# Optimization experiments

Measured on AMD Instinct MI355X. Metric: run time of the kernel, lower is better.

The kernel has to match this reference:

```python
import jax, jax.numpy as jnp
import numpy as np

NUM_ROUTES = 32 * 6 * 6  # 1152
NUM_CAPS = 10
IN_DIM = 8
OUT_DIM = 16
NUM_ITERS = 3

def _conv(x, w, stride):
    return jax.lax.conv_general_dilated(
        x, w, window_strides=(stride, stride), padding='VALID',
        dimension_numbers=('NCHW', 'OIHW', 'NCHW'))

def _squash(u):
    # squash over last axis, exactly as torch code (no eps)
    sn = (u ** 2).sum(-1, keepdims=True)
    return sn * u / ((1.0 + sn) * jnp.sqrt(sn))

def setup_inputs() -> dict:
    key = jax.random.key(0)
    ks = jax.random.split(key, 10)
    B = 512
    data = jax.random.normal(ks[0], (B, 1, 28, 28), dtype=jnp.float32)
    conv_w = jax.random.normal(ks[1], (256, 1, 9, 9), dtype=jnp.float32) * 0.05
    conv_b = jnp.zeros((256,), dtype=jnp.float32)
    # 8 primary-capsule convs stacked caps-major -> fused conv [8*32,256,9,9]
    pc_w = jax.random.normal(ks[2], (8 * 32, 256, 9, 9), dtype=jnp.float32) * 0.01
    pc_b = jnp.zeros((8 * 32,), dtype=jnp.float32)
    W = jax.random.normal(ks[3], (NUM_ROUTES, NUM_CAPS, OUT_DIM, IN_DIM), dtype=jnp.float32)
    enc_w1 = jax.random.normal(ks[4], (512, OUT_DIM * NUM_CAPS), dtype=jnp.float32) * 0.05
    enc_b1 = jnp.zeros((512,), dtype=jnp.float32)
    enc_w2 = jax.random.normal(ks[5], (9, 512), dtype=jnp.float32) * 0.05
    enc_b2 = jnp.zeros((9,), dtype=jnp.float32)
    return dict(data=data, conv_w=conv_w, conv_b=conv_b, pc_w=pc_w, pc_b=pc_b,
                W=W, enc_w1=enc_w1, enc_b1=enc_b1, enc_w2=enc_w2, enc_b2=enc_b2)

def reference(data, conv_w, conv_b, pc_w, pc_b, W, enc_w1, enc_b1, enc_w2, enc_b2):
    B = data.shape[0]
    # ConvLayer: conv + relu -> [B,256,20,20]
    x = jax.nn.relu(_conv(data, conv_w, 1) + conv_b[None, :, None, None])
    # PrimaryCaps: 8 stride-2 convs (fused, caps-major channels) -> [B,256,6,6]
    u = _conv(x, pc_w, 2) + pc_b[None, :, None, None]
    # torch: stack(dim=1) then view(B, num_routes, -1) == reshape caps-major flat
    u = u.reshape(B, NUM_ROUTES, IN_DIM)
    u = _squash(u)  # [B,R,8]
    # WaferCaps: u_hat[b,r,c,o] = sum_i W[r,c,o,i] * u[b,r,i]
    u_hat = jnp.einsum('rcoi,bri->brco', W, u)  # [B,R,C,O]
    b_ij = jnp.zeros((NUM_ROUTES, NUM_CAPS), dtype=u_hat.dtype)
    v = None
    for it in range(NUM_ITERS):
        c_ij = jax.nn.softmax(b_ij, axis=0)  # softmax over routes (dim=1 in torch)
        s = jnp.einsum('rc,brco->bco', c_ij, u_hat)  # [B,C,O]
        # original squashes [B,1,C,O,1] over last (size-1) dim -> elementwise
        s2 = s ** 2
        v = s2 * s / ((1.0 + s2) * jnp.sqrt(s2))  # = s*|s|/(1+s^2)
        if it < NUM_ITERS - 1:
            a = jnp.einsum('brco,bco->brc', u_hat, v)  # [B,R,C]
            b_ij = b_ij + a.mean(axis=0)
    # Encoder: flatten [B,C,O] row-major -> [B,160]
    flat = v.reshape(B, NUM_CAPS * OUT_DIM)
    h = jax.nn.relu(flat @ enc_w1.T + enc_b1)  # dropout is identity at eval
    out = jax.nn.sigmoid(h @ enc_w2.T + enc_b2)
    return out
```

## Files before the change

### kernel.cpp

```cpp
#include <hip/hip_runtime.h>
#include <hip/hip_bf16.h>
#include <stdint.h>


typedef __bf16 bf16_t;
typedef __bf16 bf16x4 __attribute__((ext_vector_type(4)));
typedef __bf16 bf16x8 __attribute__((ext_vector_type(8)));
typedef float f32x4 __attribute__((ext_vector_type(4)));
typedef int i32x4 __attribute__((ext_vector_type(4)));
typedef int i32x8 __attribute__((ext_vector_type(8)));

__device__ __forceinline__ void gload_lds16(const void* g, void* l) {
    __builtin_amdgcn_global_load_lds((const __attribute__((address_space(1))) void*)g,
                                     (__attribute__((address_space(3))) void*)l, 16, 0, 0);
}

#define MEMBAR() asm volatile("" ::: "memory")

__device__ __forceinline__ uint8_t fp8b(float v) {
    return (uint8_t)(__builtin_amdgcn_cvt_pk_fp8_f32(v, 0.f, 0, false) & 0xFF);
}

__global__ void k_prep(const float* __restrict__ w1, const float* __restrict__ cw,
                       float* __restrict__ w1t, bf16_t* __restrict__ Bc1,
                       float* __restrict__ bij) {
    int blk = blockIdx.x, tid = threadIdx.x;
    if (blk < 45) {
        int i = blk * 256 + tid;
        if (i < 11520) bij[i] = 0.f;
    } else if (blk < 365) {
        int i = (blk - 45) * 256 + tid;
        int j = i / 160, k = i % 160;
        w1t[k * 512 + j] = w1[i];
    } else {
        int i = (blk - 365) * 256 + tid;
        if (i < 26624) {
            int oc = i / 104, k = i % 104;
            Bc1[i] = (k < 81) ? (bf16_t)cw[oc * 81 + k] : (bf16_t)0.f;
        }
    }
}

__global__ __launch_bounds__(256) void k_w2t(const float* __restrict__ pcw,
                                             uint8_t* __restrict__ w2t8) {
    __shared__ uint16_t tmp16[10368];
    int oc = blockIdx.x, tid = threadIdx.x;
    const float* src = pcw + (size_t)oc * 20736;
    for (int q2 = tid; q2 < 10368; q2 += 256) {
        float a = src[q2 * 2] * 64.f;
        float b = src[q2 * 2 + 1] * 64.f;
        uint32_t pk = __builtin_amdgcn_cvt_pk_fp8_f32(a, b, 0, false);
        tmp16[q2] = (uint16_t)(pk & 0xFFFF);
    }
    __syncthreads();
    uint32_t* dst = (uint32_t*)(w2t8 + (size_t)oc * 20736);
    for (int w = tid; w < 5184; w += 256) {
        int k = w * 4;
        int t = k >> 8, ic0 = k & 255;
        uint32_t r = 0;
#pragma unroll
        for (int j = 0; j < 4; ++j) {
            int s = (ic0 + j) * 81 + t;
            uint32_t b = (tmp16[s >> 1] >> ((s & 1) * 8)) & 0xFF;
            r |= b << (8 * j);
        }
        dst[w] = r;
    }
}

__global__ __launch_bounds__(512) void k_c1gemm(const float* __restrict__ data,
                                                const bf16_t* __restrict__ Bc1,
                                                const float* __restrict__ cb,
                                                uint8_t* __restrict__ xt8) {
    __shared__ __align__(16) bf16_t As[128 * 104];
    __shared__ __align__(16) bf16_t Bs[256 * 104];
    __shared__ float img[1568];
    int tid = threadIdx.x, lane = tid & 63, wave = tid >> 6;
    int wm = wave >> 2, wn = wave & 3;
    for (int i = tid; i < 3328; i += 512) {
        int byte = i * 16;
        int r = byte / 208;
        int c16 = (byte - r * 208) >> 4;
        gload_lds16(Bc1 + r * 104 + c16 * 8, (char*)Bs + byte);
    }
    int mr = wm * 64 + (lane & 15);
    int nr = wn * 64 + (lane & 15);
    float bias[4];
#pragma unroll
    for (int nj = 0; nj < 4; ++nj) bias[nj] = cb[nr + nj * 16];

    for (int t = 0; t < 2; ++t) {
        int m0 = (blockIdx.x + t * 800) * 128;
        int bfirst = m0 / 400;
        int blast = (m0 + 127) / 400;
        int nimg = blast - bfirst + 1;
        __syncthreads();
        for (int i = tid; i < nimg * 784; i += 512)
            img[i] = data[(size_t)bfirst * 784 + i];
        __syncthreads();
        for (int e = tid; e < 13312; e += 512) {
            int r = e / 104, k = e - r * 104;
            int m = m0 + r;
            int b = m / 400, pos = m - b * 400;
            int oh = pos / 20, ow = pos - oh * 20;
            float x = 0.f;
            if (k < 81) {
                int kh = k / 9, kw = k - kh * 9;
                x = img[(b - bfirst) * 784 + (oh + kh) * 28 + ow + kw];
            }
            As[e] = (bf16_t)x;
        }
        asm volatile("s_waitcnt vmcnt(0)" ::: "memory");
        __syncthreads();
        f32x4 acc[4][4];
#pragma unroll
        for (int mi = 0; mi < 4; ++mi)
#pragma unroll
            for (int nj = 0; nj < 4; ++nj) acc[mi][nj] = (f32x4){0.f, 0.f, 0.f, 0.f};
#pragma unroll
        for (int kk = 0; kk < 3; ++kk) {
            int ch = (kk * 4 + (lane >> 4)) * 8;
            bf16x8 af[4], bfr[4];
#pragma unroll
            for (int i = 0; i < 4; ++i) af[i] = *(const bf16x8*)&As[(mr + i * 16) * 104 + ch];
#pragma unroll
            for (int j = 0; j < 4; ++j) bfr[j] = *(const bf16x8*)&Bs[(nr + j * 16) * 104 + ch];
#pragma unroll
            for (int mi = 0; mi < 4; ++mi)
#pragma unroll
                for (int nj = 0; nj < 4; ++nj)
                    acc[mi][nj] = __builtin_amdgcn_mfma_f32_16x16x32_bf16(af[mi], bfr[nj], acc[mi][nj], 0, 0, 0);
        }
        int mbase = m0 + wm * 64 + (lane >> 4) * 4;
#pragma unroll
        for (int mi = 0; mi < 4; ++mi)
#pragma unroll
            for (int nj = 0; nj < 4; ++nj)
#pragma unroll
                for (int j = 0; j < 4; ++j)
                    xt8[(size_t)(mbase + mi * 16 + j) * 256 + nr + nj * 16] =
                        fp8b(fmaxf(acc[mi][nj][j] + bias[nj], 0.f));
    }
}

__global__ __launch_bounds__(256) void k_pcgemm(const uint8_t* __restrict__ xt8,
                                                const uint8_t* __restrict__ w2t8,
                                                bf16_t* __restrict__ parts) {
    __shared__ __align__(16) uint8_t As[128 * 128];
    __shared__ __align__(16) uint8_t Bs[128 * 128];
    int bid = blockIdx.x;
    int mt = bid % 144;
    int nt = (bid / 144) & 1;
    int ks = bid / 288;
    int m0 = mt * 128, n0 = nt * 128;
    int tid = threadIdx.x, lane = tid & 63, wave = tid >> 6;

    int csrc = (tid & 7) ^ ((tid >> 3) & 7);
    int arow[4];
#pragma unroll
    for (int p = 0; p < 4; ++p) {
        int m = m0 + p * 32 + (tid >> 3);
        int bb = m / 36, pos = m % 36;
        int oh = pos / 6, ow = pos % 6;
        arow[p] = ((bb * 20 + oh * 2) * 20 + ow * 2) * 256;
    }
    const uint8_t* bbase = w2t8 + (size_t)(n0 + (tid >> 3)) * 20736 + csrc * 16;

    f32x4 acc[4][4];
#pragma unroll
    for (int mi = 0; mi < 4; ++mi)
#pragma unroll
        for (int ni = 0; ni < 4; ++ni) acc[mi][ni] = (f32x4){0.f, 0.f, 0.f, 0.f};

    int g0 = ks * 54;
    int mr = (wave >> 1) * 64 + (lane & 15);
    int nr = (wave & 1) * 64 + (lane & 15);
    int rx = lane & 7;
    int c0 = (2 * (lane >> 4)) ^ rx;
    int c1 = (2 * (lane >> 4) + 1) ^ rx;

    for (int it = 0; it < 54; ++it) {
        int g = g0 + it;
        int t = g >> 1, icb = g & 1;
        int kh = t / 9, kw = t - (t / 9) * 9;
        int aoff = (kh * 20 + kw) * 256 + icb * 128 + csrc * 16;
#pragma unroll
        for (int p = 0; p < 4; ++p) {
            gload_lds16(xt8 + arow[p] + aoff, &As[p * 4096 + tid * 16]);
            gload_lds16(bbase + (size_t)p * 32 * 20736 + (size_t)g * 128, &Bs[p * 4096 + tid * 16]);
        }
        __syncthreads();
        i32x8 af[4], bfr[4];
#pragma unroll
        for (int i = 0; i < 4; ++i) {
            i32x4 lo = *(const i32x4*)&As[(mr + i * 16) * 128 + c0 * 16];
            i32x4 hi = *(const i32x4*)&As[(mr + i * 16) * 128 + c1 * 16];
            af[i][0] = lo[0]; af[i][1] = lo[1]; af[i][2] = lo[2]; af[i][3] = lo[3];
            af[i][4] = hi[0]; af[i][5] = hi[1]; af[i][6] = hi[2]; af[i][7] = hi[3];
        }
#pragma unroll
        for (int i = 0; i < 4; ++i) {
            i32x4 lo = *(const i32x4*)&Bs[(nr + i * 16) * 128 + c0 * 16];
            i32x4 hi = *(const i32x4*)&Bs[(nr + i * 16) * 128 + c1 * 16];
            bfr[i][0] = lo[0]; bfr[i][1] = lo[1]; bfr[i][2] = lo[2]; bfr[i][3] = lo[3];
            bfr[i][4] = hi[0]; bfr[i][5] = hi[1]; bfr[i][6] = hi[2]; bfr[i][7] = hi[3];
        }
#pragma unroll
        for (int mi = 0; mi < 4; ++mi)
#pragma unroll
            for (int ni = 0; ni < 4; ++ni)
                acc[mi][ni] = __builtin_amdgcn_mfma_scale_f32_16x16x128_f8f6f4(
                    af[mi], bfr[ni], acc[mi][ni], 0, 0, 0, 0x7F7F7F7F, 0, 0x79797979);
        __syncthreads();
    }

    bf16_t* out = parts + (size_t)ks * 4718592;
    int mbase = m0 + (wave >> 1) * 64 + (lane >> 4) * 4;
    int nbase = n0 + (wave & 1) * 64 + (lane & 15);
#pragma unroll
    for (int mi = 0; mi < 4; ++mi)
#pragma unroll
        for (int ni = 0; ni < 4; ++ni)
#pragma unroll
            for (int j = 0; j < 4; ++j)
                out[(size_t)(mbase + mi * 16 + j) * 256 + nbase + ni * 16] = (bf16_t)acc[mi][ni][j];
}

__global__ __launch_bounds__(256) void k_squash(const bf16_t* __restrict__ parts,
                                                const float* __restrict__ pcb,
                                                bf16_t* __restrict__ ub) {
    __shared__ float s[36 * 257];
    int b = blockIdx.x, tid = threadIdx.x;
    for (int i = tid; i < 9216; i += 256) {
        float a = pcb[i & 255];
#pragma unroll
        for (int p = 0; p < 3; ++p) a += (float)parts[(size_t)p * 4718592 + (size_t)b * 9216 + i];
        s[(i >> 8) * 257 + (i & 255)] = a;
    }
    __syncthreads();
    for (int r = tid; r < 1152; r += 256) {
        int flat0 = r * 8;
        float val[8], sn = 0.f;
#pragma unroll
        for (int e = 0; e < 8; ++e) {
            int f = flat0 + e;
            float x = s[(f % 36) * 257 + f / 36];
            val[e] = x;
            sn += x * x;
        }
        float scale = sn / ((1.f + sn) * sqrtf(sn));
        bf16x8 vv;
#pragma unroll
        for (int e = 0; e < 8; ++e) vv[e] = (bf16_t)(val[e] * scale);
        *(bf16x8*)&ub[(size_t)b * 9216 + flat0] = vv;
    }
}

__global__ __launch_bounds__(256) void k_uT(const bf16_t* __restrict__ ub, bf16_t* __restrict__ uT) {
    __shared__ bf16_t t[64 * 66];
    int kt = blockIdx.x % 144, bt = blockIdx.x / 144;
    int k0 = kt * 64, b0 = bt * 64;
    int tid = threadIdx.x;
    int c8 = tid & 7;
#pragma unroll
    for (int p = 0; p < 2; ++p) {
        int r = p * 32 + (tid >> 3);
        bf16x8 vv = *(const bf16x8*)&ub[(size_t)(b0 + r) * 9216 + k0 + c8 * 8];
        uint32_t u4[4];
        *(bf16x8*)u4 = vv;
#pragma unroll
        for (int j2 = 0; j2 < 4; ++j2)
            *(uint32_t*)&t[r * 66 + c8 * 8 + j2 * 2] = u4[j2];
    }
    __syncthreads();
#pragma unroll
    for (int p = 0; p < 2; ++p) {
        int kp = p * 32 + (tid >> 3);
        bf16x8 vv;
#pragma unroll
        for (int j = 0; j < 8; ++j) vv[j] = t[(c8 * 8 + j) * 66 + kp];
        *(bf16x8*)&uT[(size_t)(k0 + kp) * 512 + b0 + c8 * 8] = vv;
    }
}

__global__ __launch_bounds__(256) void k_fold(const float* __restrict__ bij,
                                              const float* __restrict__ W,
                                              bf16_t* __restrict__ cw2T) {
    __shared__ float red[256];
    int idx0 = blockIdx.x * 256;
    int co = idx0 / 9216;
    int c = co >> 4, o = co & 15;
    int tid = threadIdx.x;
    float mx = -1e30f;
    for (int r = tid; r < 1152; r += 256) mx = fmaxf(mx, bij[r * 10 + c]);
    red[tid] = mx; __syncthreads();
    for (int s = 128; s > 0; s >>= 1) { if (tid < s) red[tid] = fmaxf(red[tid], red[tid + s]); __syncthreads(); }
    float mxv = red[0];
    __syncthreads();
    float sm = 0.f;
    for (int r = tid; r < 1152; r += 256) sm += expf(bij[r * 10 + c] - mxv);
    red[tid] = sm; __syncthreads();
    for (int s = 128; s > 0; s >>= 1) { if (tid < s) red[tid] += red[tid + s]; __syncthreads(); }
    float inv = 1.f / red[0];
    int k = (idx0 + tid) % 9216;
    int r = k >> 3, i = k & 7;
    float cij = expf(bij[r * 10 + c] - mxv) * inv;
    cw2T[idx0 + tid] = (bf16_t)(cij * W[((size_t)(r * 10 + c) * 16 + o) * 8 + i]);
}

__global__ __launch_bounds__(256) void k_rgemm(const bf16_t* __restrict__ A,
                                               const bf16_t* __restrict__ B,
                                               bf16_t* __restrict__ Cp,
                                               int Kfull, int steps, int mtiles) {
    __shared__ __align__(16) bf16_t As[64 * 64];
    __shared__ __align__(16) bf16_t Bs[160 * 64];
    int bid = blockIdx.x;
    int mt = bid % mtiles, ks = bid / mtiles;
    int m0 = mt * 64;
    int k0 = ks * steps * 64;
    int tid = threadIdx.x, lane = tid & 63, wave = tid >> 6;
    int srow = tid >> 3;
    int csrc = (tid & 7) ^ (srow & 7);
    const bf16_t* asrc[2];
    const bf16_t* bsrc[5];
#pragma unroll
    for (int p = 0; p < 2; ++p)
        asrc[p] = A + (size_t)(m0 + p * 32 + srow) * Kfull + k0 + csrc * 8;
#pragma unroll
    for (int p = 0; p < 5; ++p)
        bsrc[p] = B + (size_t)(p * 32 + srow) * Kfull + k0 + csrc * 8;

    f32x4 acc[2][5];
#pragma unroll
    for (int mi = 0; mi < 2; ++mi)
#pragma unroll
        for (int nj = 0; nj < 5; ++nj) acc[mi][nj] = (f32x4){0.f, 0.f, 0.f, 0.f};

    int mr = (wave >> 1) * 32 + (lane & 15);
    int nr = (wave & 1) * 80 + (lane & 15);
    int rx = lane & 7;

    for (int it = 0; it < steps; ++it) {
#pragma unroll
        for (int p = 0; p < 2; ++p) gload_lds16(asrc[p] + it * 64, As + p * 2048 + tid * 8);
#pragma unroll
        for (int p = 0; p < 5; ++p) gload_lds16(bsrc[p] + it * 64, Bs + p * 2048 + tid * 8);
        __syncthreads();
#pragma unroll
        for (int kk = 0; kk < 2; ++kk) {
            int ch = ((kk * 4 + (lane >> 4)) ^ rx) * 8;
            bf16x8 af[2], bfr[5];
#pragma unroll
            for (int i = 0; i < 2; ++i) af[i] = *(const bf16x8*)&As[(mr + i * 16) * 64 + ch];
#pragma unroll
            for (int j = 0; j < 5; ++j) bfr[j] = *(const bf16x8*)&Bs[(nr + j * 16) * 64 + ch];
#pragma unroll
            for (int mi = 0; mi < 2; ++mi)
#pragma unroll
                for (int nj = 0; nj < 5; ++nj)
                    acc[mi][nj] = __builtin_amdgcn_mfma_f32_16x16x32_bf16(af[mi], bfr[nj], acc[mi][nj], 0, 0, 0);
        }
        __syncthreads();
    }

    bf16_t* out = Cp + (size_t)ks * ((size_t)mtiles * 64 * 160);
    int mbase = m0 + (wave >> 1) * 32 + (lane >> 4) * 4;
    int nbase = (wave & 1) * 80 + (lane & 15);
#pragma unroll
    for (int mi = 0; mi < 2; ++mi)
#pragma unroll
        for (int nj = 0; nj < 5; ++nj)
#pragma unroll
            for (int j = 0; j < 4; ++j)
                out[(size_t)(mbase + mi * 16 + j) * 160 + nbase + nj * 16] = (bf16_t)acc[mi][nj][j];
}

__global__ void k_vcomp(const bf16_t* __restrict__ sp, float* __restrict__ v,
                        bf16_t* __restrict__ vT) {
    int idx = blockIdx.x * 256 + threadIdx.x;
    float s = 0.f;
#pragma unroll
    for (int p = 0; p < 36; ++p) s += (float)sp[(size_t)p * 81920 + idx];
    float val = s * fabsf(s) / (1.f + s * s);
    v[idx] = val;
    int b = idx / 160, co = idx % 160;
    vT[(size_t)co * 512 + b] = (bf16_t)val;
}

__global__ __launch_bounds__(256) void k_ggemm2(const bf16_t* __restrict__ uT,
                                                const bf16_t* __restrict__ vT,
                                                const float* __restrict__ W,
                                                float* __restrict__ bij) {
    __shared__ __align__(16) bf16_t As[64 * 64];
    __shared__ __align__(16) bf16_t Bs[160 * 64];
    __shared__ float Gl[64 * 161];
    int mt = blockIdx.x;
    int m0 = mt * 64;
    int tid = threadIdx.x, lane = tid & 63, wave = tid >> 6;
    int srow = tid >> 3;
    int csrc = (tid & 7) ^ (srow & 7);
    const bf16_t* asrc[2];
    const bf16_t* bsrc[5];
#pragma unroll
    for (int p = 0; p < 2; ++p)
        asrc[p] = uT + (size_t)(m0 + p * 32 + srow) * 512 + csrc * 8;
#pragma unroll
    for (int p = 0; p < 5; ++p)
        bsrc[p] = vT + (size_t)(p * 32 + srow) * 512 + csrc * 8;

    f32x4 acc[2][5];
#pragma unroll
    for (int mi = 0; mi < 2; ++mi)
#pragma unroll
        for (int nj = 0; nj < 5; ++nj) acc[mi][nj] = (f32x4){0.f, 0.f, 0.f, 0.f};

    int mr = (wave >> 1) * 32 + (lane & 15);
    int nr = (wave & 1) * 80 + (lane & 15);
    int rx = lane & 7;

    for (int it = 0; it < 8; ++it) {
#pragma unroll
        for (int p = 0; p < 2; ++p) gload_lds16(asrc[p] + it * 64, As + p * 2048 + tid * 8);
#pragma unroll
        for (int p = 0; p < 5; ++p) gload_lds16(bsrc[p] + it * 64, Bs + p * 2048 + tid * 8);
        __syncthreads();
#pragma unroll
        for (int kk = 0; kk < 2; ++kk) {
            int ch = ((kk * 4 + (lane >> 4)) ^ rx) * 8;
            bf16x8 af[2], bfr[5];
#pragma unroll
            for (int i = 0; i < 2; ++i) af[i] = *(const bf16x8*)&As[(mr + i * 16) * 64 + ch];
#pragma unroll
            for (int j = 0; j < 5; ++j) bfr[j] = *(const bf16x8*)&Bs[(nr + j * 16) * 64 + ch];
#pragma unroll
            for (int mi = 0; mi < 2; ++mi)
#pragma unroll
                for (int nj = 0; nj < 5; ++nj)
                    acc[mi][nj] = __builtin_amdgcn_mfma_f32_16x16x32_bf16(af[mi], bfr[nj], acc[mi][nj], 0, 0, 0);
        }
        __syncthreads();
    }

    int mbl = (wave >> 1) * 32 + (lane >> 4) * 4;
    int nbase = (wave & 1) * 80 + (lane & 15);
#pragma unroll
    for (int mi = 0; mi < 2; ++mi)
#pragma unroll
        for (int nj = 0; nj < 5; ++nj)
#pragma unroll
            for (int j = 0; j < 4; ++j)
                Gl[(mbl + mi * 16 + j) * 161 + nbase + nj * 16] = acc[mi][nj][j] * (1.0f / 512.0f);
    __syncthreads();
    if (tid < 80) {
        int rl = tid / 10, c = tid % 10;
        int r = mt * 8 + rl;
        const float* wbase = W + (size_t)(r * 10 + c) * 128;
        float s = 0.f;
#pragma unroll
        for (int o = 0; o < 16; ++o)
#pragma unroll
            for (int i = 0; i < 8; ++i)
                s += wbase[o * 8 + i] * Gl[(rl * 8 + i) * 161 + c * 16 + o];
        bij[r * 10 + c] += s;
    }
}

__global__ __launch_bounds__(256) void k_enc(const float* __restrict__ v,
                                             const float* __restrict__ w1t,
                                             const float* __restrict__ b1,
                                             const float* __restrict__ w2,
                                             const float* __restrict__ b2,
                                             float* __restrict__ out) {
    __shared__ float fl[160];
    __shared__ float h[512];
    int b = blockIdx.x, tid = threadIdx.x;
    if (tid < 160) fl[tid] = v[b * 160 + tid];
    __syncthreads();
    for (int j = tid; j < 512; j += 256) {
        float s = b1[j];
#pragma unroll 8
        for (int k = 0; k < 160; ++k) s += fl[k] * w1t[k * 512 + j];
        h[j] = fmaxf(s, 0.f);
    }
    __syncthreads();
    int wave = tid >> 6, lane = tid & 63;
    for (int j = wave; j < 9; j += 4) {
        float p = 0.f;
#pragma unroll
        for (int l = lane; l < 512; l += 64) p += h[l] * w2[j * 512 + l];
#pragma unroll
        for (int off = 32; off > 0; off >>= 1) p += __shfl_down(p, off, 64);
        if (lane == 0) out[b * 9 + j] = 1.f / (1.f + expf(-(p + b2[j])));
    }
}

extern "C" void kernel_launch(void* const* d_in, const int* in_sizes, int n_in,
                              void* d_out, int out_size, void* d_ws, size_t ws_size,
                              hipStream_t stream) {
    const float* data   = (const float*)d_in[0];
    const float* conv_w = (const float*)d_in[1];
    const float* conv_b = (const float*)d_in[2];
    const float* pc_w   = (const float*)d_in[3];
    const float* pc_b   = (const float*)d_in[4];
    const float* W      = (const float*)d_in[5];
    const float* enc_w1 = (const float*)d_in[6];
    const float* enc_b1 = (const float*)d_in[7];
    const float* enc_w2 = (const float*)d_in[8];
    const float* enc_b2 = (const float*)d_in[9];

    char* ws = (char*)d_ws;
    uint8_t* xt8   = (uint8_t*)(ws + 0);
    uint8_t* w2t8  = (uint8_t*)(ws + 52428800);
    bf16_t*  parts = (bf16_t*)(ws + 57737216);
    bf16_t*  uT    = (bf16_t*)(ws + 86048768);
    bf16_t*  cw2T  = (bf16_t*)(ws + 95485952);
    bf16_t*  sp    = (bf16_t*)(ws + 98435072);
    bf16_t*  ub    = (bf16_t*)(ws + 104333312);
    float*   v     = (float*)(ws + 113770496);
    bf16_t*  vT    = (bf16_t*)(ws + 114098176);
    float*   w1t   = (float*)(ws + 114262016);
    float*   bij   = (float*)(ws + 114589696);
    bf16_t*  Bc1   = (bf16_t*)(ws + 114635776);
    float*   outp  = (float*)d_out;

    hipLaunchKernelGGL(k_prep, dim3(469), dim3(256), 0, stream, enc_w1, conv_w, w1t, Bc1, bij);
    hipLaunchKernelGGL(k_w2t, dim3(256), dim3(256), 0, stream, pc_w, w2t8);
    hipLaunchKernelGGL(k_c1gemm, dim3(800), dim3(512), 0, stream, data, Bc1, conv_b, xt8);
    hipLaunchKernelGGL(k_pcgemm, dim3(864), dim3(256), 0, stream, xt8, w2t8, parts);
    hipLaunchKernelGGL(k_squash, dim3(512), dim3(256), 0, stream, parts, pc_b, ub);
    hipLaunchKernelGGL(k_uT, dim3(1152), dim3(256), 0, stream, ub, uT);
    for (int it = 0; it < 3; ++it) {
        hipLaunchKernelGGL(k_fold, dim3(5760), dim3(256), 0, stream, bij, W, cw2T);
        hipLaunchKernelGGL(k_rgemm, dim3(288), dim3(256), 0, stream, ub, cw2T, sp, 9216, 4, 8);
        hipLaunchKernelGGL(k_vcomp, dim3(320), dim3(256), 0, stream, sp, v, vT);
        if (it < 2) {
            hipLaunchKernelGGL(k_ggemm2, dim3(144), dim3(256), 0, stream, uT, vT, W, bij);
        }
    }
    hipLaunchKernelGGL(k_enc, dim3(512), dim3(256), 0, stream, v, w1t, enc_b1, enc_w2, enc_b2, outp);
}
```

Baseline: 353.6 us.

## Precompute routing softmax once, cut pcgemm split-K to two, read image directly

Adds a small k_cij kernel that computes the routing softmax once per capsule. k_fold then only multiplies c_ij by W, instead of every one of 5760 blocks redoing the max/sum reductions over 1152 routes. The primary-caps GEMM split-K goes from 3 to 2 partitions, which means fewer blocks and partial sums but longer K loops per block. The conv1 im2col now reads the input image straight from global memory instead of staging it in LDS. The extra launches per iteration and the lower parallelism in pcgemm are the trade-offs.

```diff
diff --git a/kernel.cpp b/kernel.cpp
--- a/kernel.cpp
+++ b/kernel.cpp
@@ -74,7 +74,6 @@
                                                 uint8_t* __restrict__ xt8) {
     __shared__ __align__(16) bf16_t As[128 * 104];
     __shared__ __align__(16) bf16_t Bs[256 * 104];
-    __shared__ float img[1568];
     int tid = threadIdx.x, lane = tid & 63, wave = tid >> 6;
     int wm = wave >> 2, wn = wave & 3;
     for (int i = tid; i < 3328; i += 512) {
@@ -91,12 +90,6 @@
 
     for (int t = 0; t < 2; ++t) {
         int m0 = (blockIdx.x + t * 800) * 128;
-        int bfirst = m0 / 400;
-        int blast = (m0 + 127) / 400;
-        int nimg = blast - bfirst + 1;
-        __syncthreads();
-        for (int i = tid; i < nimg * 784; i += 512)
-            img[i] = data[(size_t)bfirst * 784 + i];
         __syncthreads();
         for (int e = tid; e < 13312; e += 512) {
             int r = e / 104, k = e - r * 104;
@@ -106,7 +99,7 @@
             float x = 0.f;
             if (k < 81) {
                 int kh = k / 9, kw = k - kh * 9;
-                x = img[(b - bfirst) * 784 + (oh + kh) * 28 + ow + kw];
+                x = data[(size_t)b * 784 + (oh + kh) * 28 + ow + kw];
             }
             As[e] = (bf16_t)x;
         }
@@ -172,14 +165,14 @@
 #pragma unroll
         for (int ni = 0; ni < 4; ++ni) acc[mi][ni] = (f32x4){0.f, 0.f, 0.f, 0.f};
 
-    int g0 = ks * 54;
+    int g0 = ks * 81;
     int mr = (wave >> 1) * 64 + (lane & 15);
     int nr = (wave & 1) * 64 + (lane & 15);
     int rx = lane & 7;
     int c0 = (2 * (lane >> 4)) ^ rx;
     int c1 = (2 * (lane >> 4) + 1) ^ rx;
 
-    for (int it = 0; it < 54; ++it) {
+    for (int it = 0; it < 81; ++it) {
         int g = g0 + it;
         int t = g >> 1, icb = g & 1;
         int kh = t / 9, kw = t - (t / 9) * 9;
@@ -234,7 +227,7 @@
     for (int i = tid; i < 9216; i += 256) {
         float a = pcb[i & 255];
 #pragma unroll
-        for (int p = 0; p < 3; ++p) a += (float)parts[(size_t)p * 4718592 + (size_t)b * 9216 + i];
+        for (int p = 0; p < 2; ++p) a += (float)parts[(size_t)p * 4718592 + (size_t)b * 9216 + i];
         s[(i >> 8) * 257 + (i & 255)] = a;
     }
     __syncthreads();
@@ -283,29 +276,29 @@
     }
 }
 
-__global__ __launch_bounds__(256) void k_fold(const float* __restrict__ bij,
-                                              const float* __restrict__ W,
-                                              bf16_t* __restrict__ cw2T) {
+__global__ void k_cij(const float* __restrict__ bij, float* __restrict__ cij) {
     __shared__ float red[256];
-    int idx0 = blockIdx.x * 256;
-    int co = idx0 / 9216;
-    int c = co >> 4, o = co & 15;
-    int tid = threadIdx.x;
+    int c = blockIdx.x, tid = threadIdx.x;
     float mx = -1e30f;
     for (int r = tid; r < 1152; r += 256) mx = fmaxf(mx, bij[r * 10 + c]);
     red[tid] = mx; __syncthreads();
     for (int s = 128; s > 0; s >>= 1) { if (tid < s) red[tid] = fmaxf(red[tid], red[tid + s]); __syncthreads(); }
-    float mxv = red[0];
-    __syncthreads();
+    float MX = red[0]; __syncthreads();
     float sm = 0.f;
-    for (int r = tid; r < 1152; r += 256) sm += expf(bij[r * 10 + c] - mxv);
+    for (int r = tid; r < 1152; r += 256) sm += expf(bij[r * 10 + c] - MX);
     red[tid] = sm; __syncthreads();
     for (int s = 128; s > 0; s >>= 1) { if (tid < s) red[tid] += red[tid + s]; __syncthreads(); }
     float inv = 1.f / red[0];
-    int k = (idx0 + tid) % 9216;
+    for (int r = tid; r < 1152; r += 256) cij[r * 10 + c] = expf(bij[r * 10 + c] - MX) * inv;
+}
+
+__global__ void k_fold(const float* __restrict__ cij, const float* __restrict__ W,
+                       bf16_t* __restrict__ cw2T) {
+    int idx = blockIdx.x * 256 + threadIdx.x;
+    int co = idx / 9216, k = idx % 9216;
     int r = k >> 3, i = k & 7;
-    float cij = expf(bij[r * 10 + c] - mxv) * inv;
-    cw2T[idx0 + tid] = (bf16_t)(cij * W[((size_t)(r * 10 + c) * 16 + o) * 8 + i]);
+    int c = co >> 4, o = co & 15;
+    cw2T[idx] = (bf16_t)(cij[r * 10 + c] * W[((size_t)(r * 10 + c) * 16 + o) * 8 + i]);
 }
 
 __global__ __launch_bounds__(256) void k_rgemm(const bf16_t* __restrict__ A,
@@ -512,25 +505,27 @@
     uint8_t* xt8   = (uint8_t*)(ws + 0);
     uint8_t* w2t8  = (uint8_t*)(ws + 52428800);
     bf16_t*  parts = (bf16_t*)(ws + 57737216);
-    bf16_t*  uT    = (bf16_t*)(ws + 86048768);
-    bf16_t*  cw2T  = (bf16_t*)(ws + 95485952);
-    bf16_t*  sp    = (bf16_t*)(ws + 98435072);
-    bf16_t*  ub    = (bf16_t*)(ws + 104333312);
-    float*   v     = (float*)(ws + 113770496);
-    bf16_t*  vT    = (bf16_t*)(ws + 114098176);
-    float*   w1t   = (float*)(ws + 114262016);
-    float*   bij   = (float*)(ws + 114589696);
-    bf16_t*  Bc1   = (bf16_t*)(ws + 114635776);
+    bf16_t*  uT    = (bf16_t*)(ws + 76611584);
+    bf16_t*  cw2T  = (bf16_t*)(ws + 86048768);
+    bf16_t*  sp    = (bf16_t*)(ws + 88997888);
+    bf16_t*  ub    = (bf16_t*)(ws + 94896128);
+    float*   v     = (float*)(ws + 104333312);
+    bf16_t*  vT    = (bf16_t*)(ws + 104660992);
+    float*   w1t   = (float*)(ws + 104824832);
+    float*   bij   = (float*)(ws + 105152512);
+    float*   cij   = (float*)(ws + 105198592);
+    bf16_t*  Bc1   = (bf16_t*)(ws + 105244672);
     float*   outp  = (float*)d_out;
 
     hipLaunchKernelGGL(k_prep, dim3(469), dim3(256), 0, stream, enc_w1, conv_w, w1t, Bc1, bij);
     hipLaunchKernelGGL(k_w2t, dim3(256), dim3(256), 0, stream, pc_w, w2t8);
     hipLaunchKernelGGL(k_c1gemm, dim3(800), dim3(512), 0, stream, data, Bc1, conv_b, xt8);
-    hipLaunchKernelGGL(k_pcgemm, dim3(864), dim3(256), 0, stream, xt8, w2t8, parts);
+    hipLaunchKernelGGL(k_pcgemm, dim3(576), dim3(256), 0, stream, xt8, w2t8, parts);
     hipLaunchKernelGGL(k_squash, dim3(512), dim3(256), 0, stream, parts, pc_b, ub);
     hipLaunchKernelGGL(k_uT, dim3(1152), dim3(256), 0, stream, ub, uT);
     for (int it = 0; it < 3; ++it) {
-        hipLaunchKernelGGL(k_fold, dim3(5760), dim3(256), 0, stream, bij, W, cw2T);
+        hipLaunchKernelGGL(k_cij, dim3(10), dim3(256), 0, stream, bij, cij);
+        hipLaunchKernelGGL(k_fold, dim3(5760), dim3(256), 0, stream, cij, W, cw2T);
         hipLaunchKernelGGL(k_rgemm, dim3(288), dim3(256), 0, stream, ub, cw2T, sp, 9216, 4, 8);
         hipLaunchKernelGGL(k_vcomp, dim3(320), dim3(256), 0, stream, sp, v, vT);
         if (it < 2) {
```

After: 331.5 us. -6.2%, faster.
